# Kernel tuning notes

Hardware: AMD Instinct MI355X
Metric: run time of the kernel (lower is better)

Reference implementation:

```python
import jax, jax.numpy as jnp
import numpy as np

K = 3
STRIDE = 1
PADDING = 1


def _conv2d(x, w, b, stride, padding):
    out = jax.lax.conv_general_dilated(
        x, w, window_strides=(stride, stride),
        padding=[(padding, padding), (padding, padding)],
        dimension_numbers=('NCHW', 'OIHW', 'NCHW'))
    return out + b[None, :, None, None]


def _grid_sample_bilinear_zeros(x, grid):
    B, C, Hin, Win = x.shape
    gx = (grid[..., 0] + 1.0) * (Win * 0.5) - 0.5  # (B,Hg,Wg) pixel coords
    gy = (grid[..., 1] + 1.0) * (Hin * 0.5) - 0.5
    x0f = jnp.floor(gx)
    y0f = jnp.floor(gy)
    wx1 = gx - x0f  # bilinear weights
    wy1 = gy - y0f
    x0 = x0f.astype(jnp.int32)
    y0 = y0f.astype(jnp.int32)
    xf = x.reshape(B, C, Hin * Win)

    def gather(yi, xi):
        valid = (xi >= 0) & (xi < Win) & (yi >= 0) & (yi < Hin)  # zero padding
        idx = jnp.clip(yi, 0, Hin - 1) * Win + jnp.clip(xi, 0, Win - 1)
        g = jax.vmap(lambda xb, ib: xb[:, ib])(xf, idx)  # (B,C,Hg,Wg)
        return g * valid[:, None, :, :].astype(x.dtype)

    w00 = ((1.0 - wx1) * (1.0 - wy1))[:, None]
    w01 = (wx1 * (1.0 - wy1))[:, None]
    w10 = ((1.0 - wx1) * wy1)[:, None]
    w11 = (wx1 * wy1)[:, None]
    return (gather(y0, x0) * w00 + gather(y0, x0 + 1) * w01 +
            gather(y0 + 1, x0) * w10 + gather(y0 + 1, x0 + 1) * w11)


def setup_inputs() -> dict:
    key = jax.random.key(0)
    k1, k2, k3 = jax.random.split(key, 3)
    B, C, O, H, W = 8, 128, 128, 64, 64
    x = jax.random.normal(k1, (B, C, H, W), dtype=jnp.float32)
    # small offset-predictor weights so sampled locations stay near the grid
    w_off = jax.random.normal(k2, (2 * K * K, C, K, K), dtype=jnp.float32) * 1e-3
    b_off = jnp.zeros((2 * K * K,), dtype=jnp.float32)
    w_main = jax.random.normal(k3, (O, C, K, K), dtype=jnp.float32) * 0.05
    b_main = jnp.zeros((O,), dtype=jnp.float32)
    return {"x": x, "w_off": w_off, "b_off": b_off, "w_main": w_main, "b_main": b_main}


def reference(x, w_off, b_off, w_main, b_main):
    offset = _conv2d(x, w_off, b_off, STRIDE, PADDING)  # (B, 2*K*K, H, W)
    B, _, H, W = offset.shape
    off = jnp.transpose(offset, (0, 2, 3, 1)).reshape(B, H, W, K, K, 2)
    # The torch in-place loops reduce to:
    #   x-comp: cumsum over i of column j=0, broadcast over j
    #   y-comp: cumsum over j of row    i=0, broadcast over i
    ox = jnp.cumsum(off[:, :, :, :, 0, 0], axis=3)  # (B,H,W,K)
    oy = jnp.cumsum(off[:, :, :, 0, :, 1], axis=3)  # (B,H,W,K)
    ox_f = jnp.broadcast_to(ox[..., None], (B, H, W, K, K))
    oy_f = jnp.broadcast_to(oy[:, :, :, None, :], (B, H, W, K, K))
    off_f = jnp.stack([ox_f, oy_f], axis=-1).reshape(B, H, W, K * K, 2)

    y_range = jnp.linspace(-1.0, 1.0, H, dtype=x.dtype)
    x_range = jnp.linspace(-1.0, 1.0, W, dtype=x.dtype)
    yg, xg = jnp.meshgrid(y_range, x_range, indexing='ij')
    base = jnp.stack((xg, yg), axis=-1)  # (H,W,2)
    grid = base[None, :, :, None, :] + off_f  # (B,H,W,K*K,2)
    grid = grid.reshape(B, H, W * K * K, 2)

    xs = _grid_sample_bilinear_zeros(x, grid)  # (B,C,H,W*K*K)
    C = x.shape[1]
    xs = xs.reshape(B, C, H, W, K * K)
    wm = w_main.reshape(w_main.shape[0], C, K * K)
    out = jnp.einsum('bchwk,ock->bohw', xs, wm)
    return out + b_main[None, :, None, None]
```

## Files before the change

### kernel.cpp

```cpp
#include <hip/hip_runtime.h>
#include <hip/hip_bf16.h>
#include <stdint.h>

typedef unsigned short u16;
typedef unsigned int u32;
typedef __attribute__((ext_vector_type(8))) short short8;
typedef __attribute__((ext_vector_type(4))) float float4v;

#define CH 128
#define OO 128
#define KD 1152
#define PXT 32
#define LDB 72

__device__ __forceinline__ u16 f2bf(float v) {
    __hip_bfloat16 h = __float2bfloat16(v);
    return *reinterpret_cast<u16*>(&h);
}
__device__ __forceinline__ float bf_lo(u32 u) { u32 t = u << 16;         return __builtin_bit_cast(float, t); }
__device__ __forceinline__ float bf_hi(u32 u) { u32 t = u & 0xffff0000u; return __builtin_bit_cast(float, t); }
__device__ __forceinline__ u32 pack_bf16(float lo, float hi) {
    u32 ul = __builtin_bit_cast(u32, lo);
    u32 uh = __builtin_bit_cast(u32, hi);
    return ((ul + 0x8000u) >> 16) | ((uh + 0x8000u) & 0xffff0000u);
}

__device__ __forceinline__ uint4 sample8(const u32* __restrict__ xb, float2 g, int c8) {
    float x0f = floorf(g.x), y0f = floorf(g.y);
    float wx = g.x - x0f, wy = g.y - y0f;
    int ix0 = (int)x0f, iy0 = (int)y0f;
    int ix1 = ix0 + 1, iy1 = iy0 + 1;
    float fx0 = ((unsigned)ix0 < 64u) ? 1.f : 0.f;
    float fx1 = ((unsigned)ix1 < 64u) ? 1.f : 0.f;
    float fy0 = ((unsigned)iy0 < 64u) ? 1.f : 0.f;
    float fy1 = ((unsigned)iy1 < 64u) ? 1.f : 0.f;
    float w00 = (1.f - wy) * (1.f - wx) * fy0 * fx0;
    float w01 = (1.f - wy) * wx * fy0 * fx1;
    float w10 = wy * (1.f - wx) * fy1 * fx0;
    float w11 = wy * wx * fy1 * fx1;
    int cx0 = min(max(ix0, 0), 63), cx1 = min(max(ix1, 0), 63);
    int cy0 = min(max(iy0, 0), 63), cy1 = min(max(iy1, 0), 63);
    uint4 u00 = *(const uint4*)(xb + (((cy0 * 64 + cx0) * CH + c8) >> 1));
    uint4 u01 = *(const uint4*)(xb + (((cy0 * 64 + cx1) * CH + c8) >> 1));
    uint4 u10 = *(const uint4*)(xb + (((cy1 * 64 + cx0) * CH + c8) >> 1));
    uint4 u11 = *(const uint4*)(xb + (((cy1 * 64 + cx1) * CH + c8) >> 1));
    const u32* p00 = (const u32*)&u00;
    const u32* p01 = (const u32*)&u01;
    const u32* p10 = (const u32*)&u10;
    const u32* p11 = (const u32*)&u11;
    uint4 r;
    u32* pr = (u32*)&r;
    #pragma unroll
    for (int qq = 0; qq < 4; ++qq) {
        float lo = w00 * bf_lo(p00[qq]);
        lo = fmaf(w01, bf_lo(p01[qq]), lo);
        lo = fmaf(w10, bf_lo(p10[qq]), lo);
        lo = fmaf(w11, bf_lo(p11[qq]), lo);
        float hi = w00 * bf_hi(p00[qq]);
        hi = fmaf(w01, bf_hi(p01[qq]), hi);
        hi = fmaf(w10, bf_hi(p10[qq]), hi);
        hi = fmaf(w11, bf_hi(p11[qq]), hi);
        pr[qq] = pack_bf16(lo, hi);
    }
    return r;
}

__global__ __launch_bounds__(256) void prep_kernel(const float* __restrict__ x,
                                                   const float* __restrict__ w_off,
                                                   const float* __restrict__ w_main,
                                                   __hip_bfloat16* __restrict__ xt,
                                                   float* __restrict__ partial,
                                                   u16* __restrict__ Wb) {
    __shared__ float st[64][65];
    int bid = blockIdx.x;
    int tid = threadIdx.x;
    if (bid < 512) {
        int b = bid >> 6;
        int h = bid & 63;
        const float* xb = x + ((size_t)b * CH) * 4096 + (size_t)h * 64;
        __hip_bfloat16* xo = xt + ((size_t)bid << 6) * CH;
        for (int cc0 = 0; cc0 < 128; cc0 += 64) {
            #pragma unroll
            for (int step = 0; step < 16; ++step) {
                int cl = (tid >> 6) + step * 4;
                int w = tid & 63;
                st[cl][w] = xb[(size_t)(cc0 + cl) * 4096 + w];
            }
            __syncthreads();
            #pragma unroll
            for (int step = 0; step < 16; ++step) {
                int w = (tid >> 6) + step * 4;
                int cl = tid & 63;
                xo[(size_t)w * CH + cc0 + cl] = __float2bfloat16(st[cl][w]);
            }
            __syncthreads();
        }
    } else if (bid < 1024) {
        int mb = (bid - 512) & 127;
        int chunk = (bid - 512) >> 7;
        int m = mb * 256 + tid;
        int b = m >> 12;
        int hw = m & 4095;
        int h = hw >> 6;
        int w = hw & 63;
        float acc[6] = {0.f, 0.f, 0.f, 0.f, 0.f, 0.f};
        int c0 = chunk * 32;
        for (int c = c0; c < c0 + 32; ++c) {
            const float* xc = x + ((size_t)(b * CH + c) << 12);
            float xv[9];
            #pragma unroll
            for (int dy = 0; dy < 3; ++dy) {
                int yy = h + dy - 1;
                bool vy = (unsigned)yy < 64u;
                #pragma unroll
                for (int dx = 0; dx < 3; ++dx) {
                    int xx = w + dx - 1;
                    bool vv = vy && ((unsigned)xx < 64u);
                    xv[dy * 3 + dx] = vv ? xc[yy * 64 + xx] : 0.f;
                }
            }
            const float* wbp = w_off + (size_t)c * 9;
            #pragma unroll
            for (int s = 0; s < 6; ++s) {
                int chn = (s < 3) ? s * 6 : (s - 3) * 2 + 1;
                const float* wp = wbp + (size_t)chn * (CH * 9);
                float a = acc[s];
                #pragma unroll
                for (int t = 0; t < 9; ++t) a = fmaf(xv[t], wp[t], a);
                acc[s] = a;
            }
        }
        float* po = partial + ((size_t)(chunk << 15) + m) * 6;
        #pragma unroll
        for (int s = 0; s < 6; ++s) po[s] = acc[s];
    } else {
        int idx = (bid - 1024) * 256 + tid;
        if (idx < OO * KD) {
            int o = idx / KD;
            int r = idx - o * KD;
            int k = r >> 7;
            int c = r & 127;
            Wb[idx] = f2bf(w_main[(size_t)o * KD + c * 9 + k]);
        }
    }
}

__global__ __launch_bounds__(256, 4) void fused_gemm_kernel(const __hip_bfloat16* __restrict__ xt,
                                                            const float* __restrict__ partial,
                                                            const float* __restrict__ b_off,
                                                            const u16* __restrict__ Wb,
                                                            const float* __restrict__ b_main,
                                                            float* __restrict__ out) {
    __shared__ __align__(16) u16 lB[2][PXT * LDB];
    __shared__ float2 gxy[PXT * 9];
    __shared__ float offs[PXT * 6];

    int tid = threadIdx.x;
    int wave = tid >> 6;
    int lane = tid & 63;
    int mrow = lane & 15;
    int q8 = (lane >> 4) * 8;
    int pb = blockIdx.x * PXT;
    int bimg = pb >> 12;

    if (tid < PXT * 6) {
        int px = tid / 6, s = tid - px * 6;
        int m = pb + px;
        int chn = (s < 3) ? s * 6 : (s - 3) * 2 + 1;
        float v = b_off[chn];
        #pragma unroll
        for (int q = 0; q < 4; ++q) v += partial[((size_t)(q << 15) + m) * 6 + s];
        offs[tid] = v;
    }
    __syncthreads();
    for (int idx = tid; idx < PXT * 9; idx += 256) {
        int px = idx / 9, k = idx - px * 9;
        int i = k / 3, j = k - i * 3;
        float ox = offs[px * 6 + 0];
        if (i >= 1) ox += offs[px * 6 + 1];
        if (i >= 2) ox += offs[px * 6 + 2];
        float oy = offs[px * 6 + 3];
        if (j >= 1) oy += offs[px * 6 + 4];
        if (j >= 2) oy += offs[px * 6 + 5];
        int m = pb + px;
        int h = (m & 4095) >> 6;
        int w = m & 63;
        const float step = 2.0f / 63.0f;
        float bxn = -1.0f + w * step;
        float byn = -1.0f + h * step;
        gxy[idx] = make_float2(fmaf(bxn + ox, 32.0f, 31.5f),
                               fmaf(byn + oy, 32.0f, 31.5f));
    }
    __syncthreads();

    int spx = tid >> 3;
    int scg = tid & 7;
    const u32* xb = (const u32*)(xt + (((size_t)bimg << 12) * CH));

    {
        uint4 v = sample8(xb, gxy[spx * 9 + 0], scg * 8);
        *(uint4*)&lB[0][spx * LDB + scg * 8] = v;
    }
    __syncthreads();

    float4v acc[2][2];
    #pragma unroll
    for (int sm = 0; sm < 2; ++sm)
        #pragma unroll
        for (int sn = 0; sn < 2; ++sn)
            acc[sm][sn] = (float4v){0.f, 0.f, 0.f, 0.f};

    const u16* Wrow = Wb + (size_t)(wave * 32 + mrow) * KD;

    for (int ks = 0; ks < 18; ++ks) {
        int buf = ks & 1;
        int cbase = (ks >> 1) * 128 + (ks & 1) * 64;
        short8 af[2][2];
        #pragma unroll
        for (int sm = 0; sm < 2; ++sm)
            #pragma unroll
            for (int s = 0; s < 2; ++s)
                af[sm][s] = *(const short8*)(Wrow + (size_t)sm * 16 * KD + cbase + s * 32 + q8);
        int ksn = ks + 1;
        if (ksn < 18) {
            int k2 = ksn >> 1, ch2 = ksn & 1;
            uint4 v = sample8(xb, gxy[spx * 9 + k2], ch2 * 64 + scg * 8);
            *(uint4*)&lB[buf ^ 1][spx * LDB + scg * 8] = v;
        }
        #pragma unroll
        for (int s = 0; s < 2; ++s) {
            short8 bfv[2];
            #pragma unroll
            for (int sn = 0; sn < 2; ++sn)
                bfv[sn] = *(const short8*)&lB[buf][(sn * 16 + mrow) * LDB + s * 32 + q8];
            #pragma unroll
            for (int sm = 0; sm < 2; ++sm)
                #pragma unroll
                for (int sn = 0; sn < 2; ++sn)
                    acc[sm][sn] = __builtin_amdgcn_mfma_f32_16x16x32_bf16(af[sm][s], bfv[sn],
                                                                         acc[sm][sn], 0, 0, 0);
        }
        __syncthreads();
    }

    #pragma unroll
    for (int sm = 0; sm < 2; ++sm) {
        int o = wave * 32 + sm * 16 + (lane >> 4) * 4;
        #pragma unroll
        for (int sn = 0; sn < 2; ++sn) {
            int pcol = pb + sn * 16 + mrow;
            int rem = pcol & 4095;
            float* op = out + (((size_t)bimg * OO) << 12) + rem;
            #pragma unroll
            for (int r = 0; r < 4; ++r)
                op[(size_t)(o + r) << 12] = acc[sm][sn][r] + b_main[o + r];
        }
    }
}

extern "C" void kernel_launch(void* const* d_in, const int* in_sizes, int n_in,
                              void* d_out, int out_size, void* d_ws, size_t ws_size,
                              hipStream_t stream) {
    const float* x      = (const float*)d_in[0];
    const float* w_off  = (const float*)d_in[1];
    const float* b_off  = (const float*)d_in[2];
    const float* w_main = (const float*)d_in[3];
    const float* b_main = (const float*)d_in[4];
    float* out = (float*)d_out;

    char* ws = (char*)d_ws;
    __hip_bfloat16* xt = (__hip_bfloat16*)ws;
    float* partial = (float*)(ws + 8388608);
    u16* Wb   = (u16*)(ws + 8388608 + 3145728);

    prep_kernel<<<1600, 256, 0, stream>>>(x, w_off, w_main, xt, partial, Wb);
    fused_gemm_kernel<<<1024, 256, 0, stream>>>(xt, partial, b_off, Wb, b_main, out);
}
```

Before: 143.5 us.

## Restructure deformable GEMM: per-wave sampling into registers, swizzled weights staged in LDS

Each wave now owns 16 output pixels across all 128 output channels. It samples the bilinear B fragment straight into registers instead of staging it through a shared buffer. Per tap, the pre-swizzled bf16 weights are copied into LDS in MFMA fragment order and reused across 8 output tiles. The offset and grid computation moves into per-thread registers, which removes two block barriers and the shared offset arrays. The weight swizzle happens in the prep kernel and the grid sizes change, which trades more accumulators and lower occupancy for fewer redundant sample computations.

```diff
diff --git a/kernel.cpp b/kernel.cpp
--- a/kernel.cpp
+++ b/kernel.cpp
@@ -10,8 +10,6 @@
 #define CH 128
 #define OO 128
 #define KD 1152
-#define PXT 32
-#define LDB 72
 
 __device__ __forceinline__ u16 f2bf(float v) {
     __hip_bfloat16 h = __float2bfloat16(v);
@@ -25,52 +23,12 @@
     return ((ul + 0x8000u) >> 16) | ((uh + 0x8000u) & 0xffff0000u);
 }
 
-__device__ __forceinline__ uint4 sample8(const u32* __restrict__ xb, float2 g, int c8) {
-    float x0f = floorf(g.x), y0f = floorf(g.y);
-    float wx = g.x - x0f, wy = g.y - y0f;
-    int ix0 = (int)x0f, iy0 = (int)y0f;
-    int ix1 = ix0 + 1, iy1 = iy0 + 1;
-    float fx0 = ((unsigned)ix0 < 64u) ? 1.f : 0.f;
-    float fx1 = ((unsigned)ix1 < 64u) ? 1.f : 0.f;
-    float fy0 = ((unsigned)iy0 < 64u) ? 1.f : 0.f;
-    float fy1 = ((unsigned)iy1 < 64u) ? 1.f : 0.f;
-    float w00 = (1.f - wy) * (1.f - wx) * fy0 * fx0;
-    float w01 = (1.f - wy) * wx * fy0 * fx1;
-    float w10 = wy * (1.f - wx) * fy1 * fx0;
-    float w11 = wy * wx * fy1 * fx1;
-    int cx0 = min(max(ix0, 0), 63), cx1 = min(max(ix1, 0), 63);
-    int cy0 = min(max(iy0, 0), 63), cy1 = min(max(iy1, 0), 63);
-    uint4 u00 = *(const uint4*)(xb + (((cy0 * 64 + cx0) * CH + c8) >> 1));
-    uint4 u01 = *(const uint4*)(xb + (((cy0 * 64 + cx1) * CH + c8) >> 1));
-    uint4 u10 = *(const uint4*)(xb + (((cy1 * 64 + cx0) * CH + c8) >> 1));
-    uint4 u11 = *(const uint4*)(xb + (((cy1 * 64 + cx1) * CH + c8) >> 1));
-    const u32* p00 = (const u32*)&u00;
-    const u32* p01 = (const u32*)&u01;
-    const u32* p10 = (const u32*)&u10;
-    const u32* p11 = (const u32*)&u11;
-    uint4 r;
-    u32* pr = (u32*)&r;
-    #pragma unroll
-    for (int qq = 0; qq < 4; ++qq) {
-        float lo = w00 * bf_lo(p00[qq]);
-        lo = fmaf(w01, bf_lo(p01[qq]), lo);
-        lo = fmaf(w10, bf_lo(p10[qq]), lo);
-        lo = fmaf(w11, bf_lo(p11[qq]), lo);
-        float hi = w00 * bf_hi(p00[qq]);
-        hi = fmaf(w01, bf_hi(p01[qq]), hi);
-        hi = fmaf(w10, bf_hi(p10[qq]), hi);
-        hi = fmaf(w11, bf_hi(p11[qq]), hi);
-        pr[qq] = pack_bf16(lo, hi);
-    }
-    return r;
-}
-
 __global__ __launch_bounds__(256) void prep_kernel(const float* __restrict__ x,
                                                    const float* __restrict__ w_off,
                                                    const float* __restrict__ w_main,
                                                    __hip_bfloat16* __restrict__ xt,
                                                    float* __restrict__ partial,
-                                                   u16* __restrict__ Wb) {
+                                                   u16* __restrict__ WbSwz) {
     __shared__ float st[64][65];
     int bid = blockIdx.x;
     int tid = threadIdx.x;
@@ -134,127 +92,142 @@
         #pragma unroll
         for (int s = 0; s < 6; ++s) po[s] = acc[s];
     } else {
-        int idx = (bid - 1024) * 256 + tid;
-        if (idx < OO * KD) {
-            int o = idx / KD;
-            int r = idx - o * KD;
-            int k = r >> 7;
-            int c = r & 127;
-            Wb[idx] = f2bf(w_main[(size_t)o * KD + c * 9 + k]);
-        }
-    }
-}
-
-__global__ __launch_bounds__(256, 4) void fused_gemm_kernel(const __hip_bfloat16* __restrict__ xt,
+        int unit = (bid - 1024) * 256 + tid;
+        int lane6 = unit & 63;
+        int t = (unit >> 6) & 7;
+        int kc = unit >> 9;
+        int o = t * 16 + (lane6 & 15);
+        int q8 = (lane6 >> 4) * 8;
+        int tap = kc >> 2;
+        int cb = (kc & 3) * 32 + q8;
+        u16 v8[8];
+        #pragma unroll
+        for (int j = 0; j < 8; ++j)
+            v8[j] = f2bf(w_main[(size_t)o * KD + (cb + j) * 9 + tap]);
+        *(uint4*)(WbSwz + (size_t)unit * 8) = *(const uint4*)v8;
+    }
+}
+
+__global__ __launch_bounds__(256, 2) void fused_gemm_kernel(const __hip_bfloat16* __restrict__ xt,
                                                             const float* __restrict__ partial,
                                                             const float* __restrict__ b_off,
-                                                            const u16* __restrict__ Wb,
+                                                            const u16* __restrict__ WbSwz,
                                                             const float* __restrict__ b_main,
                                                             float* __restrict__ out) {
-    __shared__ __align__(16) u16 lB[2][PXT * LDB];
-    __shared__ float2 gxy[PXT * 9];
-    __shared__ float offs[PXT * 6];
+    __shared__ __align__(16) u16 lA[16384];
 
     int tid = threadIdx.x;
     int wave = tid >> 6;
     int lane = tid & 63;
-    int mrow = lane & 15;
+    int col = lane & 15;
     int q8 = (lane >> 4) * 8;
-    int pb = blockIdx.x * PXT;
-    int bimg = pb >> 12;
-
-    if (tid < PXT * 6) {
-        int px = tid / 6, s = tid - px * 6;
-        int m = pb + px;
+    int pbw = blockIdx.x * 64 + wave * 16;
+    int m = pbw + col;
+    int bimg = m >> 12;
+    int h = (m & 4095) >> 6;
+    int w = m & 63;
+
+    float o6[6];
+    #pragma unroll
+    for (int s = 0; s < 6; ++s) {
         int chn = (s < 3) ? s * 6 : (s - 3) * 2 + 1;
         float v = b_off[chn];
         #pragma unroll
         for (int q = 0; q < 4; ++q) v += partial[((size_t)(q << 15) + m) * 6 + s];
-        offs[tid] = v;
-    }
-    __syncthreads();
-    for (int idx = tid; idx < PXT * 9; idx += 256) {
-        int px = idx / 9, k = idx - px * 9;
-        int i = k / 3, j = k - i * 3;
-        float ox = offs[px * 6 + 0];
-        if (i >= 1) ox += offs[px * 6 + 1];
-        if (i >= 2) ox += offs[px * 6 + 2];
-        float oy = offs[px * 6 + 3];
-        if (j >= 1) oy += offs[px * 6 + 4];
-        if (j >= 2) oy += offs[px * 6 + 5];
-        int m = pb + px;
-        int h = (m & 4095) >> 6;
-        int w = m & 63;
-        const float step = 2.0f / 63.0f;
-        float bxn = -1.0f + w * step;
-        float byn = -1.0f + h * step;
-        gxy[idx] = make_float2(fmaf(bxn + ox, 32.0f, 31.5f),
-                               fmaf(byn + oy, 32.0f, 31.5f));
-    }
-    __syncthreads();
-
-    int spx = tid >> 3;
-    int scg = tid & 7;
+        o6[s] = v;
+    }
+    float ox0 = o6[0], ox1 = ox0 + o6[1], ox2 = ox1 + o6[2];
+    float oy0 = o6[3], oy1 = oy0 + o6[4], oy2 = oy1 + o6[5];
+    const float step = 2.0f / 63.0f;
+    float bxn = -1.0f + w * step;
+    float byn = -1.0f + h * step;
+    float gx0 = fmaf(bxn + ox0, 32.0f, 31.5f);
+    float gx1 = fmaf(bxn + ox1, 32.0f, 31.5f);
+    float gx2 = fmaf(bxn + ox2, 32.0f, 31.5f);
+    float gy0 = fmaf(byn + oy0, 32.0f, 31.5f);
+    float gy1 = fmaf(byn + oy1, 32.0f, 31.5f);
+    float gy2 = fmaf(byn + oy2, 32.0f, 31.5f);
+
     const u32* xb = (const u32*)(xt + (((size_t)bimg << 12) * CH));
 
-    {
-        uint4 v = sample8(xb, gxy[spx * 9 + 0], scg * 8);
-        *(uint4*)&lB[0][spx * LDB + scg * 8] = v;
-    }
-    __syncthreads();
-
-    float4v acc[2][2];
+    float4v acc[8];
     #pragma unroll
-    for (int sm = 0; sm < 2; ++sm)
-        #pragma unroll
-        for (int sn = 0; sn < 2; ++sn)
-            acc[sm][sn] = (float4v){0.f, 0.f, 0.f, 0.f};
-
-    const u16* Wrow = Wb + (size_t)(wave * 32 + mrow) * KD;
-
-    for (int ks = 0; ks < 18; ++ks) {
-        int buf = ks & 1;
-        int cbase = (ks >> 1) * 128 + (ks & 1) * 64;
-        short8 af[2][2];
-        #pragma unroll
-        for (int sm = 0; sm < 2; ++sm)
-            #pragma unroll
-            for (int s = 0; s < 2; ++s)
-                af[sm][s] = *(const short8*)(Wrow + (size_t)sm * 16 * KD + cbase + s * 32 + q8);
-        int ksn = ks + 1;
-        if (ksn < 18) {
-            int k2 = ksn >> 1, ch2 = ksn & 1;
-            uint4 v = sample8(xb, gxy[spx * 9 + k2], ch2 * 64 + scg * 8);
-            *(uint4*)&lB[buf ^ 1][spx * LDB + scg * 8] = v;
+    for (int t = 0; t < 8; ++t) acc[t] = (float4v){0.f, 0.f, 0.f, 0.f};
+
+    for (int tap = 0; tap < 9; ++tap) {
+        __syncthreads();
+        const uint4* s4 = (const uint4*)(WbSwz + (size_t)tap * 16384);
+        uint4* d4 = (uint4*)lA;
+        #pragma unroll
+        for (int it = 0; it < 8; ++it) d4[it * 256 + tid] = s4[it * 256 + tid];
+        __syncthreads();
+
+        float gxi = (tap >= 6) ? gx2 : ((tap >= 3) ? gx1 : gx0);
+        int jm = tap - ((tap >= 6) ? 6 : ((tap >= 3) ? 3 : 0));
+        float gyj = (jm == 2) ? gy2 : ((jm == 1) ? gy1 : gy0);
+        float x0f = floorf(gxi), y0f = floorf(gyj);
+        float wx = gxi - x0f, wy = gyj - y0f;
+        int ix0 = (int)x0f, iy0 = (int)y0f;
+        int ix1 = ix0 + 1, iy1 = iy0 + 1;
+        float fx0 = ((unsigned)ix0 < 64u) ? 1.f : 0.f;
+        float fx1 = ((unsigned)ix1 < 64u) ? 1.f : 0.f;
+        float fy0 = ((unsigned)iy0 < 64u) ? 1.f : 0.f;
+        float fy1 = ((unsigned)iy1 < 64u) ? 1.f : 0.f;
+        float w00 = (1.f - wy) * (1.f - wx) * fy0 * fx0;
+        float w01 = (1.f - wy) * wx * fy0 * fx1;
+        float w10 = wy * (1.f - wx) * fy1 * fx0;
+        float w11 = wy * wx * fy1 * fx1;
+        int cx0 = min(max(ix0, 0), 63), cx1 = min(max(ix1, 0), 63);
+        int cy0 = min(max(iy0, 0), 63), cy1 = min(max(iy1, 0), 63);
+        int r00 = (cy0 * 64 + cx0) * CH + q8;
+        int r01 = (cy0 * 64 + cx1) * CH + q8;
+        int r10 = (cy1 * 64 + cx0) * CH + q8;
+        int r11 = (cy1 * 64 + cx1) * CH + q8;
+
+        #pragma unroll
+        for (int cc = 0; cc < 4; ++cc) {
+            int co = cc * 16;
+            uint4 u00 = *(const uint4*)(xb + (r00 >> 1) + co);
+            uint4 u01 = *(const uint4*)(xb + (r01 >> 1) + co);
+            uint4 u10 = *(const uint4*)(xb + (r10 >> 1) + co);
+            uint4 u11 = *(const uint4*)(xb + (r11 >> 1) + co);
+            const u32* p00 = (const u32*)&u00;
+            const u32* p01 = (const u32*)&u01;
+            const u32* p10 = (const u32*)&u10;
+            const u32* p11 = (const u32*)&u11;
+            u32 bp[4];
+            #pragma unroll
+            for (int qq = 0; qq < 4; ++qq) {
+                float lo = w00 * bf_lo(p00[qq]);
+                lo = fmaf(w01, bf_lo(p01[qq]), lo);
+                lo = fmaf(w10, bf_lo(p10[qq]), lo);
+                lo = fmaf(w11, bf_lo(p11[qq]), lo);
+                float hi = w00 * bf_hi(p00[qq]);
+                hi = fmaf(w01, bf_hi(p01[qq]), hi);
+                hi = fmaf(w10, bf_hi(p10[qq]), hi);
+                hi = fmaf(w11, bf_hi(p11[qq]), hi);
+                bp[qq] = pack_bf16(lo, hi);
+            }
+            short8 bfrag = *(const short8*)bp;
+            #pragma unroll
+            for (int t = 0; t < 8; ++t) {
+                short8 af = *(const short8*)&lA[((cc * 8 + t) * 64 + lane) * 8];
+                acc[t] = __builtin_amdgcn_mfma_f32_16x16x32_bf16(af, bfrag, acc[t], 0, 0, 0);
+            }
         }
-        #pragma unroll
-        for (int s = 0; s < 2; ++s) {
-            short8 bfv[2];
-            #pragma unroll
-            for (int sn = 0; sn < 2; ++sn)
-                bfv[sn] = *(const short8*)&lB[buf][(sn * 16 + mrow) * LDB + s * 32 + q8];
-            #pragma unroll
-            for (int sm = 0; sm < 2; ++sm)
-                #pragma unroll
-                for (int sn = 0; sn < 2; ++sn)
-                    acc[sm][sn] = __builtin_amdgcn_mfma_f32_16x16x32_bf16(af[sm][s], bfv[sn],
-                                                                         acc[sm][sn], 0, 0, 0);
-        }
-        __syncthreads();
-    }
-
+    }
+
+    int quad4 = (lane >> 4) * 4;
+    int rem = m & 4095;
     #pragma unroll
-    for (int sm = 0; sm < 2; ++sm) {
-        int o = wave * 32 + sm * 16 + (lane >> 4) * 4;
-        #pragma unroll
-        for (int sn = 0; sn < 2; ++sn) {
-            int pcol = pb + sn * 16 + mrow;
-            int rem = pcol & 4095;
-            float* op = out + (((size_t)bimg * OO) << 12) + rem;
-            #pragma unroll
-            for (int r = 0; r < 4; ++r)
-                op[(size_t)(o + r) << 12] = acc[sm][sn][r] + b_main[o + r];
-        }
+    for (int t = 0; t < 8; ++t) {
+        int ob = t * 16 + quad4;
+        float4 bm = *(const float4*)(b_main + ob);
+        float* op = out + (((size_t)(bimg * OO + ob)) << 12) + rem;
+        op[0] = acc[t][0] + bm.x;
+        op[4096] = acc[t][1] + bm.y;
+        op[8192] = acc[t][2] + bm.z;
+        op[12288] = acc[t][3] + bm.w;
     }
 }
 
@@ -271,8 +244,8 @@
     char* ws = (char*)d_ws;
     __hip_bfloat16* xt = (__hip_bfloat16*)ws;
     float* partial = (float*)(ws + 8388608);
-    u16* Wb   = (u16*)(ws + 8388608 + 3145728);
-
-    prep_kernel<<<1600, 256, 0, stream>>>(x, w_off, w_main, xt, partial, Wb);
-    fused_gemm_kernel<<<1024, 256, 0, stream>>>(xt, partial, b_off, Wb, b_main, out);
-}
+    u16* WbSwz = (u16*)(ws + 8388608 + 3145728);
+
+    prep_kernel<<<1096, 256, 0, stream>>>(x, w_off, w_main, xt, partial, WbSwz);
+    fused_gemm_kernel<<<512, 256, 0, stream>>>(xt, partial, b_off, WbSwz, b_main, out);
+}
```

Result: no change. 141.1 us (-1.7%).
